# Kernel tuning notes

Measured on AMD Instinct MI355X. Metric: run time of the kernel, lower is better.

The kernel has to match this reference:

```python
import jax, jax.numpy as jnp
import numpy as np

N_BINS = 15


def setup_inputs() -> dict:
    key = jax.random.key(0)
    k1, k2 = jax.random.split(key)
    logits = jax.random.normal(k1, (1000000, 256), dtype=jnp.float32)
    labels = jax.random.randint(k2, (1000000,), 0, 256, dtype=jnp.int64)
    return {"logits": logits, "labels": labels}


def reference(logits, labels):
    # softmax -> per-sample confidence (max prob) and prediction (argmax)
    probs = jax.nn.softmax(logits, axis=-1)
    confidences = jnp.max(probs, axis=-1)            # [N]
    predictions = jnp.argmax(probs, axis=-1)         # [N]
    accuracies = (predictions == labels).astype(logits.dtype)

    # Bin i covers (i/n_bins, (i+1)/n_bins]: searchsorted(side='left') - 1.
    boundaries = jnp.linspace(0.0, 1.0, N_BINS + 1, dtype=logits.dtype)
    bin_idx = jnp.clip(jnp.searchsorted(boundaries, confidences, side="left") - 1, 0, N_BINS - 1)

    n = confidences.shape[0]
    counts = jax.ops.segment_sum(jnp.ones_like(confidences), bin_idx, num_segments=N_BINS)
    conf_sum = jax.ops.segment_sum(confidences, bin_idx, num_segments=N_BINS)
    acc_sum = jax.ops.segment_sum(accuracies, bin_idx, num_segments=N_BINS)

    safe_counts = jnp.maximum(counts, 1.0)
    gap = jnp.abs(conf_sum / safe_counts - acc_sum / safe_counts)   # |avg_conf - acc| per bin
    ece = jnp.sum(jnp.where(counts > 0, gap * counts / n, 0.0))
    return ece.reshape(1)
```

## Files before the change

kernel.cpp:

```cpp
#include <hip/hip_runtime.h>

#define N_BINS 15
#define WS_FLOATS (3 * N_BINS)
#define ROWS 4

__global__ void ece_zero_ws(float* __restrict__ ws) {
    int i = threadIdx.x;
    if (i < WS_FLOATS) ws[i] = 0.0f;
}

__global__ __launch_bounds__(256) void ece_main(const float* __restrict__ logits,
                                                const int* __restrict__ labels,
                                                float* __restrict__ ws,
                                                int n_rows) {
    __shared__ float sbins[WS_FLOATS];
    for (int i = threadIdx.x; i < WS_FLOATS; i += blockDim.x) sbins[i] = 0.0f;
    __syncthreads();

    const int lane = threadIdx.x & 63;
    const int g    = lane >> 4;
    const int t    = lane & 15;
    const int wv   = threadIdx.x >> 6;
    const int wpb  = blockDim.x >> 6;
    const long long gwave  = (long long)blockIdx.x * wpb + wv;
    const long long nwaves = (long long)gridDim.x * wpb;
    const long long step   = nwaves * ROWS;

    for (long long base = gwave * ROWS; base < n_rows; base += step) {
        const long long r = base + g;
        const bool valid = (r < n_rows);

        float4 v0, v1, v2, v3;
        if (valid) {
            const float4* p = reinterpret_cast<const float4*>(logits) + (r << 6) + (t << 2);
            v0 = p[0]; v1 = p[1]; v2 = p[2]; v3 = p[3];
        } else {
            v0 = v1 = v2 = v3 = make_float4(-1e30f, -1e30f, -1e30f, -1e30f);
        }

        float m = fmaxf(fmaxf(fmaxf(v0.x, v0.y), fmaxf(v0.z, v0.w)),
                        fmaxf(fmaxf(v1.x, v1.y), fmaxf(v1.z, v1.w)));
        m = fmaxf(m, fmaxf(fmaxf(fmaxf(v2.x, v2.y), fmaxf(v2.z, v2.w)),
                           fmaxf(fmaxf(v3.x, v3.y), fmaxf(v3.z, v3.w))));

        float s = ((__expf(v0.x) + __expf(v0.y)) + (__expf(v0.z) + __expf(v0.w)))
                + ((__expf(v1.x) + __expf(v1.y)) + (__expf(v1.z) + __expf(v1.w)))
                + ((__expf(v2.x) + __expf(v2.y)) + (__expf(v2.z) + __expf(v2.w)))
                + ((__expf(v3.x) + __expf(v3.y)) + (__expf(v3.z) + __expf(v3.w)));

        #pragma unroll
        for (int off = 8; off >= 1; off >>= 1) {
            m = fmaxf(m, __shfl_xor(m, off));
            s += __shfl_xor(s, off);
        }

        if (t == 0 && valid) {
            const int   lab       = labels[r];
            const float lab_logit = logits[(r << 8) + lab];
            const float conf      = __expf(m) / s;
            const float acc       = (lab_logit == m) ? 1.0f : 0.0f;

            int left = 0;
            #pragma unroll
            for (int j = 0; j <= N_BINS; ++j) {
                float b = (float)((double)j * (1.0 / 15.0));
                if (j == N_BINS) b = 1.0f;
                left += (b < conf) ? 1 : 0;
            }
            int bin = left - 1;
            bin = bin < 0 ? 0 : (bin > N_BINS - 1 ? N_BINS - 1 : bin);

            atomicAdd(&sbins[bin], 1.0f);
            atomicAdd(&sbins[N_BINS + bin], conf);
            atomicAdd(&sbins[2 * N_BINS + bin], acc);
        }
    }

    __syncthreads();
    for (int i = threadIdx.x; i < WS_FLOATS; i += blockDim.x) {
        const float val = sbins[i];
        if (val != 0.0f) atomicAdd(&ws[i], val);
    }
}

__global__ void ece_final(const float* __restrict__ ws, float* __restrict__ out, float n) {
    float ece = 0.0f;
    for (int i = 0; i < N_BINS; ++i) {
        const float c = ws[i];
        if (c > 0.0f) {
            const float sc  = c < 1.0f ? 1.0f : c;
            const float gap = fabsf(ws[N_BINS + i] / sc - ws[2 * N_BINS + i] / sc);
            ece += gap * c / n;
        }
    }
    out[0] = ece;
}

extern "C" void kernel_launch(void* const* d_in, const int* in_sizes, int n_in,
                              void* d_out, int out_size, void* d_ws, size_t ws_size,
                              hipStream_t stream) {
    const float* logits = (const float*)d_in[0];
    const int*   labels = (const int*)d_in[1];
    float* out = (float*)d_out;
    float* ws  = (float*)d_ws;
    const int n_rows = in_sizes[1];

    ece_zero_ws<<<1, 64, 0, stream>>>(ws);
    ece_main<<<2048, 256, 0, stream>>>(logits, labels, ws, n_rows);
    ece_final<<<1, 1, 0, stream>>>(ws, out, (float)n_rows);
}
```

Measured before the change: 187.8 us.

## Replace global atomics with per-block partials and select label logit in registers

When the workspace is large enough, each block writes its bin statistics to a per-block partials array, and a 1024-thread final kernel reduces them. This removes the zero-init launch and the global atomics. The label logit is now picked from the already-loaded registers with a select tree and a ballot, so the dependent scattered global load per row goes away. If the workspace is too small, the old atomic path is kept as a fallback. The cost is a larger workspace write and a heavier final reduction.

Result: slower. 192.5 us (+2.5%).

```diff
diff --git a/kernel.cpp b/kernel.cpp
--- a/kernel.cpp
+++ b/kernel.cpp
@@ -1,20 +1,17 @@
 #include <hip/hip_runtime.h>
 
 #define N_BINS 15
-#define WS_FLOATS (3 * N_BINS)
-#define ROWS 4
-
-__global__ void ece_zero_ws(float* __restrict__ ws) {
-    int i = threadIdx.x;
-    if (i < WS_FLOATS) ws[i] = 0.0f;
-}
-
-__global__ __launch_bounds__(256) void ece_main(const float* __restrict__ logits,
-                                                const int* __restrict__ labels,
-                                                float* __restrict__ ws,
-                                                int n_rows) {
-    __shared__ float sbins[WS_FLOATS];
-    for (int i = threadIdx.x; i < WS_FLOATS; i += blockDim.x) sbins[i] = 0.0f;
+#define NSTATS (3 * N_BINS)
+#define NBLK   2048
+#define ROWS   4
+
+
+__global__ __launch_bounds__(256) void ece_main_p(const float* __restrict__ logits,
+                                                  const int* __restrict__ labels,
+                                                  float* __restrict__ partials,
+                                                  int n_rows) {
+    __shared__ float sbins[NSTATS];
+    for (int i = threadIdx.x; i < NSTATS; i += blockDim.x) sbins[i] = 0.0f;
     __syncthreads();
 
     const int lane = threadIdx.x & 63;
@@ -31,9 +28,11 @@
         const bool valid = (r < n_rows);
 
         float4 v0, v1, v2, v3;
+        int lab = 0;
         if (valid) {
             const float4* p = reinterpret_cast<const float4*>(logits) + (r << 6) + (t << 2);
             v0 = p[0]; v1 = p[1]; v2 = p[2]; v3 = p[3];
+            lab = labels[r];
         } else {
             v0 = v1 = v2 = v3 = make_float4(-1e30f, -1e30f, -1e30f, -1e30f);
         }
@@ -48,17 +47,28 @@
                 + ((__expf(v2.x) + __expf(v2.y)) + (__expf(v2.z) + __expf(v2.w)))
                 + ((__expf(v3.x) + __expf(v3.y)) + (__expf(v3.z) + __expf(v3.w)));
 
+        const bool b0 = lab & 1, b1 = lab & 2, b2 = lab & 4, b3 = lab & 8;
+        const float s01 = b0 ? v0.y : v0.x, s23 = b0 ? v0.w : v0.z;
+        const float s45 = b0 ? v1.y : v1.x, s67 = b0 ? v1.w : v1.z;
+        const float s89 = b0 ? v2.y : v2.x, sAB = b0 ? v2.w : v2.z;
+        const float sCD = b0 ? v3.y : v3.x, sEF = b0 ? v3.w : v3.z;
+        const float t0 = b1 ? s23 : s01, t1 = b1 ? s67 : s45;
+        const float t2 = b1 ? sAB : s89, t3 = b1 ? sEF : sCD;
+        const float u0 = b2 ? t1 : t0,  u1 = b2 ? t3 : t2;
+        const float sel = b3 ? u1 : u0;
+        const bool owner = ((lab >> 4) == t);
+
         #pragma unroll
         for (int off = 8; off >= 1; off >>= 1) {
             m = fmaxf(m, __shfl_xor(m, off));
             s += __shfl_xor(s, off);
         }
 
+        const unsigned long long mask = __ballot(valid && owner && (sel == m));
+
         if (t == 0 && valid) {
-            const int   lab       = labels[r];
-            const float lab_logit = logits[(r << 8) + lab];
-            const float conf      = __expf(m) / s;
-            const float acc       = (lab_logit == m) ? 1.0f : 0.0f;
+            const float conf = __expf(m) / s;
+            const float acc  = ((mask >> (g << 4)) & 0xFFFFULL) ? 1.0f : 0.0f;
 
             int left = 0;
             #pragma unroll
@@ -77,13 +87,109 @@
     }
 
     __syncthreads();
-    for (int i = threadIdx.x; i < WS_FLOATS; i += blockDim.x) {
+    for (int i = threadIdx.x; i < NSTATS; i += blockDim.x)
+        partials[i * NBLK + blockIdx.x] = sbins[i];
+}
+
+__global__ __launch_bounds__(1024) void ece_final_p(const float* __restrict__ partials,
+                                                    float* __restrict__ out, float n) {
+    __shared__ float stat[NSTATS];
+    const int wv   = threadIdx.x >> 6;
+    const int lane = threadIdx.x & 63;
+    for (int s = wv; s < NSTATS; s += 16) {
+        float acc = 0.0f;
+        #pragma unroll 4
+        for (int b = lane; b < NBLK; b += 64) acc += partials[s * NBLK + b];
+        #pragma unroll
+        for (int off = 32; off >= 1; off >>= 1) acc += __shfl_xor(acc, off);
+        if (lane == 0) stat[s] = acc;
+    }
+    __syncthreads();
+    if (threadIdx.x == 0) {
+        float ece = 0.0f;
+        for (int i = 0; i < N_BINS; ++i) {
+            const float c = stat[i];
+            if (c > 0.0f) {
+                const float sc  = c < 1.0f ? 1.0f : c;
+                const float gap = fabsf(stat[N_BINS + i] / sc - stat[2 * N_BINS + i] / sc);
+                ece += gap * c / n;
+            }
+        }
+        out[0] = ece;
+    }
+}
+
+
+__global__ void ece_zero_ws(float* __restrict__ ws) {
+    int i = threadIdx.x;
+    if (i < NSTATS) ws[i] = 0.0f;
+}
+
+__global__ __launch_bounds__(256) void ece_main_a(const float* __restrict__ logits,
+                                                  const int* __restrict__ labels,
+                                                  float* __restrict__ ws,
+                                                  int n_rows) {
+    __shared__ float sbins[NSTATS];
+    for (int i = threadIdx.x; i < NSTATS; i += blockDim.x) sbins[i] = 0.0f;
+    __syncthreads();
+
+    const int lane = threadIdx.x & 63;
+    const int g = lane >> 4, t = lane & 15;
+    const int wv = threadIdx.x >> 6, wpb = blockDim.x >> 6;
+    const long long gwave  = (long long)blockIdx.x * wpb + wv;
+    const long long nwaves = (long long)gridDim.x * wpb;
+    const long long step   = nwaves * ROWS;
+
+    for (long long base = gwave * ROWS; base < n_rows; base += step) {
+        const long long r = base + g;
+        const bool valid = (r < n_rows);
+        float4 v0, v1, v2, v3;
+        if (valid) {
+            const float4* p = reinterpret_cast<const float4*>(logits) + (r << 6) + (t << 2);
+            v0 = p[0]; v1 = p[1]; v2 = p[2]; v3 = p[3];
+        } else {
+            v0 = v1 = v2 = v3 = make_float4(-1e30f, -1e30f, -1e30f, -1e30f);
+        }
+        float m = fmaxf(fmaxf(fmaxf(v0.x, v0.y), fmaxf(v0.z, v0.w)),
+                        fmaxf(fmaxf(v1.x, v1.y), fmaxf(v1.z, v1.w)));
+        m = fmaxf(m, fmaxf(fmaxf(fmaxf(v2.x, v2.y), fmaxf(v2.z, v2.w)),
+                           fmaxf(fmaxf(v3.x, v3.y), fmaxf(v3.z, v3.w))));
+        float s = ((__expf(v0.x) + __expf(v0.y)) + (__expf(v0.z) + __expf(v0.w)))
+                + ((__expf(v1.x) + __expf(v1.y)) + (__expf(v1.z) + __expf(v1.w)))
+                + ((__expf(v2.x) + __expf(v2.y)) + (__expf(v2.z) + __expf(v2.w)))
+                + ((__expf(v3.x) + __expf(v3.y)) + (__expf(v3.z) + __expf(v3.w)));
+        #pragma unroll
+        for (int off = 8; off >= 1; off >>= 1) {
+            m = fmaxf(m, __shfl_xor(m, off));
+            s += __shfl_xor(s, off);
+        }
+        if (t == 0 && valid) {
+            const int lab = labels[r];
+            const float lab_logit = logits[(r << 8) + lab];
+            const float conf = __expf(m) / s;
+            const float acc  = (lab_logit == m) ? 1.0f : 0.0f;
+            int left = 0;
+            #pragma unroll
+            for (int j = 0; j <= N_BINS; ++j) {
+                float b = (float)((double)j * (1.0 / 15.0));
+                if (j == N_BINS) b = 1.0f;
+                left += (b < conf) ? 1 : 0;
+            }
+            int bin = left - 1;
+            bin = bin < 0 ? 0 : (bin > N_BINS - 1 ? N_BINS - 1 : bin);
+            atomicAdd(&sbins[bin], 1.0f);
+            atomicAdd(&sbins[N_BINS + bin], conf);
+            atomicAdd(&sbins[2 * N_BINS + bin], acc);
+        }
+    }
+    __syncthreads();
+    for (int i = threadIdx.x; i < NSTATS; i += blockDim.x) {
         const float val = sbins[i];
         if (val != 0.0f) atomicAdd(&ws[i], val);
     }
 }
 
-__global__ void ece_final(const float* __restrict__ ws, float* __restrict__ out, float n) {
+__global__ void ece_final_a(const float* __restrict__ ws, float* __restrict__ out, float n) {
     float ece = 0.0f;
     for (int i = 0; i < N_BINS; ++i) {
         const float c = ws[i];
@@ -95,6 +201,7 @@
     }
     out[0] = ece;
 }
+
 
 extern "C" void kernel_launch(void* const* d_in, const int* in_sizes, int n_in,
                               void* d_out, int out_size, void* d_ws, size_t ws_size,
@@ -105,7 +212,13 @@
     float* ws  = (float*)d_ws;
     const int n_rows = in_sizes[1];
 
-    ece_zero_ws<<<1, 64, 0, stream>>>(ws);
-    ece_main<<<2048, 256, 0, stream>>>(logits, labels, ws, n_rows);
-    ece_final<<<1, 1, 0, stream>>>(ws, out, (float)n_rows);
-}
+    const size_t needed = (size_t)NSTATS * NBLK * sizeof(float);
+    if (ws_size >= needed) {
+        ece_main_p<<<NBLK, 256, 0, stream>>>(logits, labels, ws, n_rows);
+        ece_final_p<<<1, 1024, 0, stream>>>(ws, out, (float)n_rows);
+    } else {
+        ece_zero_ws<<<1, 64, 0, stream>>>(ws);
+        ece_main_a<<<NBLK, 256, 0, stream>>>(logits, labels, ws, n_rows);
+        ece_final_a<<<1, 1, 0, stream>>>(ws, out, (float)n_rows);
+    }
+}
```
